# Performance work log

Hardware: AMD Instinct MI355X
Metric: run time of the kernel (lower is better)

Reference implementation:

```python
import jax, jax.numpy as jnp
import numpy as np

T, B, D, H = 1024, 8, 1024, 16

def setup_inputs() -> dict:
    key = jax.random.key(0)
    ks = jax.random.split(key, 9)
    s = 0.02
    return {
        "x": jax.random.normal(ks[0], (T, B, D), dtype=jnp.float32),
        "Wq": jax.random.normal(ks[1], (D, D), dtype=jnp.float32) * s,
        "bq": jnp.zeros((D,), dtype=jnp.float32),
        "Wk": jax.random.normal(ks[2], (D, D), dtype=jnp.float32) * s,
        "bk": jnp.zeros((D,), dtype=jnp.float32),
        "Wv": jax.random.normal(ks[3], (D, D), dtype=jnp.float32) * s,
        "bv": jnp.zeros((D,), dtype=jnp.float32),
        "Wo": jax.random.normal(ks[4], (D, D), dtype=jnp.float32) * s,
        "bo": jnp.zeros((D,), dtype=jnp.float32),
        "n_heads": H,
    }

def reference(x, Wq, bq, Wk, bk, Wv, bv, Wo, bo, n_heads):
    t, b, D = x.shape
    h = n_heads
    d = D // h
    scale = 1.0 / jnp.sqrt(jnp.float32(d))
    # nn.Linear: y = x @ W.T + b
    q = (x @ Wq.T + bq).reshape(t, b, h, d)
    k = (x @ Wk.T + bk).reshape(t, b, h, d)
    v = (x @ Wv.T + bv).reshape(t, b, h, d)
    # scores: [b, h, t_query, t_key]
    scores = jnp.einsum('tbhd,sbhd->bhts', q, k) * scale
    attn = jax.nn.softmax(scores, axis=-1)
    out = jnp.einsum('bhts,sbhd->tbhd', attn, v).reshape(t, b, D)
    return out @ Wo.T + bo
```

## Files before the change

### kernel.cpp

```cpp
#include <hip/hip_runtime.h>


#define Tn 1024
#define Bn 8
#define Dn 1024
#define Hn 16
#define HDn 64
#define Mn 8192
#define Kn 1024

typedef float f32x4 __attribute__((ext_vector_type(4)));
typedef __bf16 bf16x8 __attribute__((ext_vector_type(8)));
typedef unsigned short u16x8 __attribute__((ext_vector_type(8)));
typedef unsigned short u16x4 __attribute__((ext_vector_type(4)));

#define GLL16(g, l)                                                        \
  __builtin_amdgcn_global_load_lds(                                        \
      (const __attribute__((address_space(1))) void*)(g),                  \
      (__attribute__((address_space(3))) void*)(l), 16, 0, 0)

__device__ __forceinline__ unsigned short f2bf(float f) {
  unsigned int u = __float_as_uint(f);
  u += 0x7fffu + ((u >> 16) & 1u);
  return (unsigned short)(u >> 16);
}

__device__ __forceinline__ unsigned short bfbits(float f) {
  __bf16 h = (__bf16)f;
  return __builtin_bit_cast(unsigned short, h);
}

__global__ __launch_bounds__(256) void cvt_kernel(
    const float* __restrict__ src, unsigned short* __restrict__ dst, int n4) {
  int i = blockIdx.x * 256 + threadIdx.x;
  const int stride = gridDim.x * 256;
  for (; i < n4; i += stride) {
    const float4 v = ((const float4*)src)[i];
    u16x4 o;
    o.x = f2bf(v.x); o.y = f2bf(v.y); o.z = f2bf(v.z); o.w = f2bf(v.w);
    ((u16x4*)dst)[i] = o;
  }
}

__global__ __launch_bounds__(256) void cvt4_kernel(
    const float* __restrict__ s0, const float* __restrict__ s1,
    const float* __restrict__ s2, const float* __restrict__ s3,
    unsigned short* __restrict__ d0, unsigned short* __restrict__ d1,
    unsigned short* __restrict__ d2, unsigned short* __restrict__ d3, int n4) {
  const int z = blockIdx.z;
  const float* src = (z == 0) ? s0 : (z == 1) ? s1 : (z == 2) ? s2 : s3;
  unsigned short* dst = (z == 0) ? d0 : (z == 1) ? d1 : (z == 2) ? d2 : d3;
  int i = blockIdx.x * 256 + threadIdx.x;
  const int stride = gridDim.x * 256;
  for (; i < n4; i += stride) {
    const float4 v = ((const float4*)src)[i];
    u16x4 o;
    o.x = f2bf(v.x); o.y = f2bf(v.y); o.z = f2bf(v.z); o.w = f2bf(v.w);
    ((u16x4*)dst)[i] = o;
  }
}

__device__ __forceinline__ void gemm128_core(
    const unsigned short* __restrict__ A, const unsigned short* __restrict__ Bw,
    unsigned short* lds_a, unsigned short* lds_b, int bm, int bn,
    f32x4 acc[4][4]) {
  const int tid = threadIdx.x;
  const int lane = tid & 63;
  const int w = tid >> 6;
  const int wr = w >> 1, wc = w & 1;
  const int fr = lane & 15, fg = lane >> 4;

  const int p0 = tid, p1 = tid + 256;
  const int r0 = p0 >> 2, c0 = (p0 & 3) ^ ((r0 ^ (r0 >> 2)) & 3);
  const int r1 = p1 >> 2, c1 = (p1 & 3) ^ ((r1 ^ (r1 >> 2)) & 3);
  const unsigned short* gA0 = A + (size_t)(bm * 128 + r0) * Kn + c0 * 8;
  const unsigned short* gA1 = A + (size_t)(bm * 128 + r1) * Kn + c1 * 8;
  const unsigned short* gB0 = Bw + (size_t)(bn * 128 + r0) * Kn + c0 * 8;
  const unsigned short* gB1 = Bw + (size_t)(bn * 128 + r1) * Kn + c1 * 8;

  int aoff[4], boff[4];
#pragma unroll
  for (int m = 0; m < 4; m++) {
    const int row = wr * 64 + m * 16 + fr;
    aoff[m] = row * 32 + ((fg ^ ((row ^ (row >> 2)) & 3)) * 8);
  }
#pragma unroll
  for (int n = 0; n < 4; n++) {
    const int row = wc * 64 + n * 16 + fr;
    boff[n] = row * 32 + ((fg ^ ((row ^ (row >> 2)) & 3)) * 8);
  }

  for (int k0 = 0; k0 < Kn; k0 += 32) {
    GLL16(gA0 + k0, &lds_a[tid * 8]);
    GLL16(gA1 + k0, &lds_a[(tid + 256) * 8]);
    GLL16(gB0 + k0, &lds_b[tid * 8]);
    GLL16(gB1 + k0, &lds_b[(tid + 256) * 8]);
    __syncthreads();
    bf16x8 af[4], bfr[4];
#pragma unroll
    for (int m = 0; m < 4; m++) af[m] = *(const bf16x8*)&lds_a[aoff[m]];
#pragma unroll
    for (int n = 0; n < 4; n++) bfr[n] = *(const bf16x8*)&lds_b[boff[n]];
#pragma unroll
    for (int m = 0; m < 4; m++)
#pragma unroll
      for (int n = 0; n < 4; n++)
        acc[m][n] = __builtin_amdgcn_mfma_f32_16x16x32_bf16(af[m], bfr[n],
                                                            acc[m][n], 0, 0, 0);
    __syncthreads();
  }
}

__global__ __launch_bounds__(256) void gemm_qkv(
    const unsigned short* __restrict__ xbf, const unsigned short* __restrict__ wq,
    const unsigned short* __restrict__ wk, const unsigned short* __restrict__ wv,
    const float* __restrict__ bq, const float* __restrict__ bk,
    const float* __restrict__ bv, unsigned short* __restrict__ qd,
    unsigned short* __restrict__ kd, unsigned short* __restrict__ vd) {
  __shared__ __align__(16) unsigned short lds_a[128 * 32];
  __shared__ __align__(16) unsigned short lds_b[128 * 32];
  const int z = blockIdx.z;
  const unsigned short* Bw = (z == 0) ? wq : (z == 1) ? wk : wv;
  const float* bias = (z == 0) ? bq : (z == 1) ? bk : bv;
  unsigned short* dst = (z == 0) ? qd : (z == 1) ? kd : vd;
  const float sc = (z == 0) ? 0.125f * 1.44269504088896f : 1.0f;

  f32x4 acc[4][4] = {};
  gemm128_core(xbf, Bw, lds_a, lds_b, blockIdx.x, blockIdx.y, acc);

  const int tid = threadIdx.x, lane = tid & 63, w = tid >> 6;
  const int wr = w >> 1, wc = w & 1, fr = lane & 15, fg = lane >> 4;
#pragma unroll
  for (int n = 0; n < 4; n++) {
    const int gcol = blockIdx.y * 128 + wc * 64 + n * 16 + fr;
    const float bc = bias[gcol];
    const int hh = gcol >> 6, dd = gcol & 63;
#pragma unroll
    for (int m = 0; m < 4; m++) {
      const int rowbase = blockIdx.x * 128 + wr * 64 + m * 16 + fg * 4;
#pragma unroll
      for (int r = 0; r < 4; r++) {
        const int grow = rowbase + r;
        const int tt = grow >> 3, bb = grow & 7;
        const float v = (acc[m][n][r] + bc) * sc;
        dst[((size_t)(bb * Hn + hh) * Tn + tt) * HDn + dd] = f2bf(v);
      }
    }
  }
}

__global__ __launch_bounds__(256) void gemm_out(
    const unsigned short* __restrict__ abf, const unsigned short* __restrict__ wo,
    const float* __restrict__ bo, float* __restrict__ out) {
  __shared__ __align__(16) unsigned short lds_a[128 * 32];
  __shared__ __align__(16) unsigned short lds_b[128 * 32];
  f32x4 acc[4][4] = {};
  gemm128_core(abf, wo, lds_a, lds_b, blockIdx.x, blockIdx.y, acc);

  const int tid = threadIdx.x, lane = tid & 63, w = tid >> 6;
  const int wr = w >> 1, wc = w & 1, fr = lane & 15, fg = lane >> 4;
#pragma unroll
  for (int n = 0; n < 4; n++) {
    const int gcol = blockIdx.y * 128 + wc * 64 + n * 16 + fr;
    const float bc = bo[gcol];
#pragma unroll
    for (int m = 0; m < 4; m++) {
      const int rowbase = blockIdx.x * 128 + wr * 64 + m * 16 + fg * 4;
#pragma unroll
      for (int r = 0; r < 4; r++) {
        const int grow = rowbase + r;
        out[(size_t)grow * Dn + gcol] = acc[m][n][r] + bc;
      }
    }
  }
}

__global__ __launch_bounds__(256) void transpose_v(
    const unsigned short* __restrict__ src, unsigned short* __restrict__ dst) {
  __shared__ unsigned short tile[64][72];
  const int tid = threadIdx.x;
  const size_t base = (size_t)blockIdx.y * ((size_t)Tn * HDn);
  const int t0 = blockIdx.x * 64;
#pragma unroll
  for (int it = 0; it < 2; it++) {
    const int p = it * 256 + tid;
    const int r = p >> 3, c = (p & 7) * 8;
    *(u16x8*)&tile[r][c] =
        *(const u16x8*)(src + base + (size_t)(t0 + r) * HDn + c);
  }
  __syncthreads();
#pragma unroll
  for (int it = 0; it < 2; it++) {
    const int p = it * 256 + tid;
    const int d = p >> 3, tc = (p & 7) * 8;
    u16x8 v;
#pragma unroll
    for (int j = 0; j < 8; j++) v[j] = tile[tc + j][d];
    *(u16x8*)(dst + base + (size_t)d * Tn + t0 + tc) = v;
  }
}

__global__ __launch_bounds__(256) void attn_fwd(
    const unsigned short* __restrict__ Q, const unsigned short* __restrict__ K,
    const unsigned short* __restrict__ Vt, unsigned short* __restrict__ Ob) {
  __shared__ __align__(16) unsigned short k2[2][64 * 64];
  __shared__ __align__(16) unsigned short v2[2][64 * 64];
  __shared__ __align__(16) unsigned short p_all[64 * 64];

  const int tid = threadIdx.x, lane = tid & 63, w = tid >> 6;
  const int fr = lane & 15, fg = lane >> 4;
  const int bh = blockIdx.x;
  const int qt = blockIdx.y;
  const int bb = bh >> 4, hh = bh & 15;

  const unsigned short* Qbh = Q + (size_t)bh * (Tn * HDn);
  const unsigned short* Kbh = K + (size_t)bh * (Tn * HDn);
  const unsigned short* Vbh = Vt + (size_t)bh * (HDn * Tn);

  const int p0 = tid, p1 = tid + 256;
  const int r0 = p0 >> 3, c0 = (p0 & 7) ^ (r0 & 7);
  const int r1 = p1 >> 3, c1 = (p1 & 7) ^ (r1 & 7);

  GLL16(Qbh + (size_t)(qt * 64 + r0) * HDn + c0 * 8, &p_all[p0 * 8]);
  GLL16(Qbh + (size_t)(qt * 64 + r1) * HDn + c1 * 8, &p_all[p1 * 8]);
  __syncthreads();
  bf16x8 qa[2];
#pragma unroll
  for (int ks = 0; ks < 2; ks++) {
    const int row = w * 16 + fr;
    const int blk = (ks * 4 + fg) ^ (row & 7);
    qa[ks] = *(const bf16x8*)&p_all[row * 64 + blk * 8];
  }

  bf16x8 vones;
#pragma unroll
  for (int j = 0; j < 8; j++) vones[j] = (__bf16)1.0f;

#define STAGE_KV(nx, bi)                                                     \
  do {                                                                       \
    GLL16(Kbh + (size_t)((nx) * 64 + r0) * HDn + c0 * 8, &k2[bi][p0 * 8]);   \
    GLL16(Kbh + (size_t)((nx) * 64 + r1) * HDn + c1 * 8, &k2[bi][p1 * 8]);   \
    GLL16(Vbh + (size_t)r0 * Tn + (nx) * 64 + c0 * 8, &v2[bi][p0 * 8]);      \
    GLL16(Vbh + (size_t)r1 * Tn + (nx) * 64 + c1 * 8, &v2[bi][p1 * 8]);      \
  } while (0)

  STAGE_KV(0, 0);
  __syncthreads();

  f32x4 o[4] = {};
  float lsum[4] = {};
  const float FM = 12.0f;

  for (int kt = 0; kt < 16; kt++) {
    const int cur = kt & 1;
    if (kt < 15) STAGE_KV(kt + 1, cur ^ 1);
    const unsigned short* kl = k2[cur];
    const unsigned short* vl = v2[cur];

    f32x4 s[4] = {};
    __builtin_amdgcn_s_setprio(1);
#pragma unroll
    for (int n = 0; n < 4; n++)
#pragma unroll
      for (int ks = 0; ks < 2; ks++) {
        const int krow = n * 16 + fr;
        const int blk = (ks * 4 + fg) ^ (krow & 7);
        const bf16x8 kb = *(const bf16x8*)&kl[krow * 64 + blk * 8];
        s[n] = __builtin_amdgcn_mfma_f32_16x16x32_bf16(kb, qa[ks], s[n], 0, 0, 0);
      }
    __builtin_amdgcn_s_setprio(0);

#pragma unroll
    for (int n = 0; n < 4; n++) {
      u16x4 pk;
#pragma unroll
      for (int r = 0; r < 4; r++) pk[r] = bfbits(exp2f(s[n][r] - FM));
      const int addr = (w * 16 + fr) * 64 +
                       (((2 * n + (fg >> 1)) ^ (fr & 7)) * 8) + (fg & 1) * 4;
      *(u16x4*)&p_all[addr] = pk;
    }

    bf16x8 pa[2];
#pragma unroll
    for (int ks = 0; ks < 2; ks++) {
      const int blk = (ks * 4 + fg) ^ (fr & 7);
      pa[ks] = *(const bf16x8*)&p_all[(w * 16 + fr) * 64 + blk * 8];
    }

    f32x4 ss = {};
    ss = __builtin_amdgcn_mfma_f32_16x16x32_bf16(pa[0], vones, ss, 0, 0, 0);
    ss = __builtin_amdgcn_mfma_f32_16x16x32_bf16(pa[1], vones, ss, 0, 0, 0);
#pragma unroll
    for (int r = 0; r < 4; r++) lsum[r] += ss[r];

    __builtin_amdgcn_s_setprio(1);
#pragma unroll
    for (int ks = 0; ks < 2; ks++)
#pragma unroll
      for (int n = 0; n < 4; n++) {
        const int vrow = n * 16 + fr;
        const int vblk = (ks * 4 + fg) ^ (vrow & 7);
        const bf16x8 vb = *(const bf16x8*)&vl[vrow * 64 + vblk * 8];
        o[n] = __builtin_amdgcn_mfma_f32_16x16x32_bf16(pa[ks], vb, o[n], 0, 0, 0);
      }
    __builtin_amdgcn_s_setprio(0);
    __syncthreads();
  }
#undef STAGE_KV

#pragma unroll
  for (int r = 0; r < 4; r++) lsum[r] = 1.0f / lsum[r];
  const int tbase = qt * 64 + w * 16 + fg * 4;
#pragma unroll
  for (int n = 0; n < 4; n++) {
    const int dcol = n * 16 + fr;
#pragma unroll
    for (int r = 0; r < 4; r++) {
      const int tt = tbase + r;
      const float val = o[n][r] * lsum[r];
      Ob[((size_t)(tt * Bn + bb)) * Dn + hh * HDn + dcol] = bfbits(val);
    }
  }
}

extern "C" void kernel_launch(void* const* d_in, const int* in_sizes, int n_in,
                              void* d_out, int out_size, void* d_ws,
                              size_t ws_size, hipStream_t stream) {
  (void)in_sizes; (void)n_in; (void)out_size; (void)ws_size;
  const float* x  = (const float*)d_in[0];
  const float* Wq = (const float*)d_in[1];
  const float* bq = (const float*)d_in[2];
  const float* Wk = (const float*)d_in[3];
  const float* bk = (const float*)d_in[4];
  const float* Wv = (const float*)d_in[5];
  const float* bv = (const float*)d_in[6];
  const float* Wo = (const float*)d_in[7];
  const float* bo = (const float*)d_in[8];
  float* out = (float*)d_out;

  unsigned short* ws  = (unsigned short*)d_ws;
  unsigned short* xbf = ws;
  unsigned short* wqb = xbf + (size_t)Mn * Kn;
  unsigned short* wkb = wqb + (size_t)Dn * Dn;
  unsigned short* wvb = wkb + (size_t)Dn * Dn;
  unsigned short* wob = wvb + (size_t)Dn * Dn;
  unsigned short* qb  = wob + (size_t)Dn * Dn;
  unsigned short* kb  = qb + (size_t)Mn * Dn;
  unsigned short* vb  = kb + (size_t)Mn * Dn;
  unsigned short* vtb = xbf;
  unsigned short* ab  = vb;

  cvt_kernel<<<1024, 256, 0, stream>>>(x, xbf, Mn * Kn / 4);
  cvt4_kernel<<<dim3(256, 1, 4), 256, 0, stream>>>(
      Wq, Wk, Wv, Wo, wqb, wkb, wvb, wob, Dn * Dn / 4);

  gemm_qkv<<<dim3(Mn / 128, Dn / 128, 3), 256, 0, stream>>>(
      xbf, wqb, wkb, wvb, bq, bk, bv, qb, kb, vb);
  transpose_v<<<dim3(Tn / 64, Bn * Hn), 256, 0, stream>>>(vb, vtb);
  attn_fwd<<<dim3(Bn * Hn, Tn / 64), 256, 0, stream>>>(qb, kb, vtb, ab);
  gemm_out<<<dim3(Mn / 128, Dn / 128), 256, 0, stream>>>(ab, wob, bo, out);
}
```

Before: 270.8 us.

## Double-buffer GEMM LDS tiles and merge conversion kernels into one launch

Splits the shared GEMM core's LDS into two stages so the next K-tile's global-to-LDS loads are issued before the current tile's MFMAs run, removing one barrier per iteration. Merges the input and four weight fp32-to-bf16 conversions into a single launch. This doubles LDS per block, which can reduce occupancy, and gives the x conversion fewer blocks.

```diff
diff --git a/kernel.cpp b/kernel.cpp
--- a/kernel.cpp
+++ b/kernel.cpp
@@ -30,8 +30,21 @@
   return __builtin_bit_cast(unsigned short, h);
 }
 
-__global__ __launch_bounds__(256) void cvt_kernel(
-    const float* __restrict__ src, unsigned short* __restrict__ dst, int n4) {
+__global__ __launch_bounds__(256) void cvt_all(
+    const float* __restrict__ x, const float* __restrict__ s0,
+    const float* __restrict__ s1, const float* __restrict__ s2,
+    const float* __restrict__ s3, unsigned short* __restrict__ dx,
+    unsigned short* __restrict__ d0, unsigned short* __restrict__ d1,
+    unsigned short* __restrict__ d2, unsigned short* __restrict__ d3) {
+  const int z = blockIdx.z;
+  const float* src;
+  unsigned short* dst;
+  int n4;
+  if (z == 0)      { src = x;  dst = dx; n4 = Mn * Kn / 4; }
+  else if (z == 1) { src = s0; dst = d0; n4 = Dn * Dn / 4; }
+  else if (z == 2) { src = s1; dst = d1; n4 = Dn * Dn / 4; }
+  else if (z == 3) { src = s2; dst = d2; n4 = Dn * Dn / 4; }
+  else             { src = s3; dst = d3; n4 = Dn * Dn / 4; }
   int i = blockIdx.x * 256 + threadIdx.x;
   const int stride = gridDim.x * 256;
   for (; i < n4; i += stride) {
@@ -42,28 +55,10 @@
   }
 }
 
-__global__ __launch_bounds__(256) void cvt4_kernel(
-    const float* __restrict__ s0, const float* __restrict__ s1,
-    const float* __restrict__ s2, const float* __restrict__ s3,
-    unsigned short* __restrict__ d0, unsigned short* __restrict__ d1,
-    unsigned short* __restrict__ d2, unsigned short* __restrict__ d3, int n4) {
-  const int z = blockIdx.z;
-  const float* src = (z == 0) ? s0 : (z == 1) ? s1 : (z == 2) ? s2 : s3;
-  unsigned short* dst = (z == 0) ? d0 : (z == 1) ? d1 : (z == 2) ? d2 : d3;
-  int i = blockIdx.x * 256 + threadIdx.x;
-  const int stride = gridDim.x * 256;
-  for (; i < n4; i += stride) {
-    const float4 v = ((const float4*)src)[i];
-    u16x4 o;
-    o.x = f2bf(v.x); o.y = f2bf(v.y); o.z = f2bf(v.z); o.w = f2bf(v.w);
-    ((u16x4*)dst)[i] = o;
-  }
-}
-
 __device__ __forceinline__ void gemm128_core(
     const unsigned short* __restrict__ A, const unsigned short* __restrict__ Bw,
-    unsigned short* lds_a, unsigned short* lds_b, int bm, int bn,
-    f32x4 acc[4][4]) {
+    unsigned short* lds_a, unsigned short* lds_b,
+    int bm, int bn, f32x4 acc[4][4]) {
   const int tid = threadIdx.x;
   const int lane = tid & 63;
   const int w = tid >> 6;
@@ -90,17 +85,27 @@
     boff[n] = row * 32 + ((fg ^ ((row ^ (row >> 2)) & 3)) * 8);
   }
 
-  for (int k0 = 0; k0 < Kn; k0 += 32) {
-    GLL16(gA0 + k0, &lds_a[tid * 8]);
-    GLL16(gA1 + k0, &lds_a[(tid + 256) * 8]);
-    GLL16(gB0 + k0, &lds_b[tid * 8]);
-    GLL16(gB1 + k0, &lds_b[(tid + 256) * 8]);
-    __syncthreads();
+#define GSTAGE(koff, bi)                                                  \
+  do {                                                                    \
+    GLL16(gA0 + (koff), &lds_a[(bi) * 4096 + tid * 8]);                   \
+    GLL16(gA1 + (koff), &lds_a[(bi) * 4096 + (tid + 256) * 8]);           \
+    GLL16(gB0 + (koff), &lds_b[(bi) * 4096 + tid * 8]);                   \
+    GLL16(gB1 + (koff), &lds_b[(bi) * 4096 + (tid + 256) * 8]);           \
+  } while (0)
+
+  GSTAGE(0, 0);
+  __syncthreads();
+
+  for (int kk = 0; kk < 32; ++kk) {
+    const int cur = kk & 1;
+    if (kk < 31) GSTAGE((kk + 1) * 32, cur ^ 1);
+    const unsigned short* la = lds_a + cur * 4096;
+    const unsigned short* lb = lds_b + cur * 4096;
     bf16x8 af[4], bfr[4];
 #pragma unroll
-    for (int m = 0; m < 4; m++) af[m] = *(const bf16x8*)&lds_a[aoff[m]];
-#pragma unroll
-    for (int n = 0; n < 4; n++) bfr[n] = *(const bf16x8*)&lds_b[boff[n]];
+    for (int m = 0; m < 4; m++) af[m] = *(const bf16x8*)&la[aoff[m]];
+#pragma unroll
+    for (int n = 0; n < 4; n++) bfr[n] = *(const bf16x8*)&lb[boff[n]];
 #pragma unroll
     for (int m = 0; m < 4; m++)
 #pragma unroll
@@ -109,6 +114,7 @@
                                                             acc[m][n], 0, 0, 0);
     __syncthreads();
   }
+#undef GSTAGE
 }
 
 __global__ __launch_bounds__(256) void gemm_qkv(
@@ -117,8 +123,8 @@
     const float* __restrict__ bq, const float* __restrict__ bk,
     const float* __restrict__ bv, unsigned short* __restrict__ qd,
     unsigned short* __restrict__ kd, unsigned short* __restrict__ vd) {
-  __shared__ __align__(16) unsigned short lds_a[128 * 32];
-  __shared__ __align__(16) unsigned short lds_b[128 * 32];
+  __shared__ __align__(16) unsigned short lds_a[2 * 128 * 32];
+  __shared__ __align__(16) unsigned short lds_b[2 * 128 * 32];
   const int z = blockIdx.z;
   const unsigned short* Bw = (z == 0) ? wq : (z == 1) ? wk : wv;
   const float* bias = (z == 0) ? bq : (z == 1) ? bk : bv;
@@ -152,8 +158,8 @@
 __global__ __launch_bounds__(256) void gemm_out(
     const unsigned short* __restrict__ abf, const unsigned short* __restrict__ wo,
     const float* __restrict__ bo, float* __restrict__ out) {
-  __shared__ __align__(16) unsigned short lds_a[128 * 32];
-  __shared__ __align__(16) unsigned short lds_b[128 * 32];
+  __shared__ __align__(16) unsigned short lds_a[2 * 128 * 32];
+  __shared__ __align__(16) unsigned short lds_b[2 * 128 * 32];
   f32x4 acc[4][4] = {};
   gemm128_core(abf, wo, lds_a, lds_b, blockIdx.x, blockIdx.y, acc);
 
@@ -350,9 +356,8 @@
   unsigned short* vtb = xbf;
   unsigned short* ab  = vb;
 
-  cvt_kernel<<<1024, 256, 0, stream>>>(x, xbf, Mn * Kn / 4);
-  cvt4_kernel<<<dim3(256, 1, 4), 256, 0, stream>>>(
-      Wq, Wk, Wv, Wo, wqb, wkb, wvb, wob, Dn * Dn / 4);
+  cvt_all<<<dim3(512, 1, 5), 256, 0, stream>>>(
+      x, Wq, Wk, Wv, Wo, xbf, wqb, wkb, wvb, wob);
 
   gemm_qkv<<<dim3(Mn / 128, Dn / 128, 3), 256, 0, stream>>>(
       xbf, wqb, wkb, wvb, bq, bk, bv, qb, kb, vb);
```

Result: slower. 290.2 us (+7.2%).
